# Optimization experiments

Hardware: AMD Instinct MI355X
Metric: run time of the kernel (lower is better)

## Reference

```python
import jax, jax.numpy as jnp
import numpy as np

C = 512

def setup_inputs() -> dict:
    key = jax.random.key(0)
    ks = jax.random.split(key, 7)
    x = jax.random.normal(ks[0], (4, C, 64, 64), dtype=jnp.float32)
    s = 1.0 / np.sqrt(C)
    f_w = jax.random.normal(ks[1], (C // 2, C), dtype=jnp.float32) * s
    f_b = jax.random.normal(ks[2], (C // 2,), dtype=jnp.float32) * 0.01
    g_w = jax.random.normal(ks[3], (C // 2, C), dtype=jnp.float32) * s
    g_b = jax.random.normal(ks[4], (C // 2,), dtype=jnp.float32) * 0.01
    h_w = jax.random.normal(ks[5], (C, C), dtype=jnp.float32) * s
    h_b = jax.random.normal(ks[6], (C,), dtype=jnp.float32) * 0.01
    return {"x": x, "f_w": f_w, "f_b": f_b, "g_w": g_w, "g_b": g_b, "h_w": h_w, "h_b": h_b}

def reference(x, f_w, f_b, g_w, g_b, h_w, h_b):
    B, Cc, H, W = x.shape
    N = H * W
    xf = x.reshape(B, Cc, N)  # hw_flatten
    # 1x1 convs are channel GEMMs: [B,Cout,N]
    f = jnp.einsum('oc,bcn->bon', f_w, xf) + f_b[None, :, None]
    g = jnp.einsum('oc,bcn->bon', g_w, xf) + g_b[None, :, None]
    h = jnp.einsum('oc,bcn->bon', h_w, xf) + h_b[None, :, None]
    # energy[b,i,j] = sum_k f[b,k,i] * g[b,k,j]
    energy = jnp.einsum('bki,bkj->bij', f, g)
    attention = jax.nn.softmax(energy, axis=-1)
    # ret[b,c,i] = sum_j h[b,c,j] * attention[b,i,j]
    ret = jnp.einsum('bcj,bij->bci', h, attention)
    return ret.reshape(B, Cc, H, W)
```

## Files before the change

kernel.cpp:

```cpp
#include <hip/hip_runtime.h>


#define NPIX 4096
#define CIN  512

typedef _Float16 f16x4 __attribute__((ext_vector_type(4)));
typedef _Float16 f16x8 __attribute__((ext_vector_type(8)));
typedef float    f32x4 __attribute__((ext_vector_type(4)));
typedef float    f32x16 __attribute__((ext_vector_type(16)));

#define MFMA16(a, b, c) __builtin_amdgcn_mfma_f32_16x16x16f16(a, b, c, 0, 0, 0)
#define MFMA32(a, b, c) __builtin_amdgcn_mfma_f32_32x32x16_f16(a, b, c, 0, 0, 0)

__device__ __forceinline__ void gld_lds16(const void* g, void* l) {
    __builtin_amdgcn_global_load_lds(
        (const __attribute__((address_space(1))) unsigned int*)g,
        (__attribute__((address_space(3))) unsigned int*)l, 16, 0, 0);
}

__global__ __launch_bounds__(256) void proj_kernel(
    const float* __restrict__ x,
    const float* __restrict__ f_w, const float* __restrict__ f_b,
    const float* __restrict__ g_w, const float* __restrict__ g_b,
    const float* __restrict__ h_w, const float* __restrict__ h_b,
    _Float16* __restrict__ qw, _Float16* __restrict__ kw,
    _Float16* __restrict__ vw)
{
    const int b  = blockIdx.z;
    const int n0 = blockIdx.x * 64;
    const int o0 = blockIdx.y * 64;

    const float* wsrc; const float* bsrc;
    if (o0 < 256)      { wsrc = f_w + (size_t)o0 * CIN;         bsrc = f_b + o0; }
    else if (o0 < 512) { wsrc = g_w + (size_t)(o0 - 256) * CIN; bsrc = g_b + (o0 - 256); }
    else               { wsrc = h_w + (size_t)(o0 - 512) * CIN; bsrc = h_b + (o0 - 512); }

    __shared__ _Float16 Wt[64][40];
    __shared__ _Float16 Xt[64][40];

    const int t = threadIdx.x;
    const int lane = t & 63, wv = t >> 6;
    const int wm = wv >> 1, wn = wv & 1;
    const int gi = lane >> 4, li = lane & 15;

    f32x4 acc[2][2];
    #pragma unroll
    for (int i = 0; i < 2; ++i)
        #pragma unroll
        for (int j = 0; j < 2; ++j) acc[i][j] = f32x4{0.f, 0.f, 0.f, 0.f};

    for (int kk = 0; kk < CIN; kk += 32) {
        {
            const int r = t >> 2, c8 = (t & 3) * 8;
            const float* p = wsrc + (size_t)r * CIN + kk + c8;
            const float4 v0 = *(const float4*)p;
            const float4 v1 = *(const float4*)(p + 4);
            _Float16* d = &Wt[r][c8];
            d[0] = (_Float16)v0.x; d[1] = (_Float16)v0.y;
            d[2] = (_Float16)v0.z; d[3] = (_Float16)v0.w;
            d[4] = (_Float16)v1.x; d[5] = (_Float16)v1.y;
            d[6] = (_Float16)v1.z; d[7] = (_Float16)v1.w;
        }
        {
            const int c = t >> 3, n8 = (t & 7) * 8;
            const float* p = x + ((size_t)b * CIN + kk + c) * NPIX + n0 + n8;
            const float4 v0 = *(const float4*)p;
            const float4 v1 = *(const float4*)(p + 4);
            Xt[n8 + 0][c] = (_Float16)v0.x; Xt[n8 + 1][c] = (_Float16)v0.y;
            Xt[n8 + 2][c] = (_Float16)v0.z; Xt[n8 + 3][c] = (_Float16)v0.w;
            Xt[n8 + 4][c] = (_Float16)v1.x; Xt[n8 + 5][c] = (_Float16)v1.y;
            Xt[n8 + 6][c] = (_Float16)v1.z; Xt[n8 + 7][c] = (_Float16)v1.w;
        }
        __syncthreads();
        #pragma unroll
        for (int kh = 0; kh < 2; ++kh) {
            const int ko = kh * 16 + gi * 4;
            f16x4 a0 = *(const f16x4*)&Wt[wm * 32 +      li][ko];
            f16x4 a1 = *(const f16x4*)&Wt[wm * 32 + 16 + li][ko];
            f16x4 b0 = *(const f16x4*)&Xt[wn * 32 +      li][ko];
            f16x4 b1 = *(const f16x4*)&Xt[wn * 32 + 16 + li][ko];
            acc[0][0] = MFMA16(a0, b0, acc[0][0]);
            acc[0][1] = MFMA16(a0, b1, acc[0][1]);
            acc[1][0] = MFMA16(a1, b0, acc[1][0]);
            acc[1][1] = MFMA16(a1, b1, acc[1][1]);
        }
        __syncthreads();
    }

    #pragma unroll
    for (int mf = 0; mf < 2; ++mf)
        #pragma unroll
        for (int nf = 0; nf < 2; ++nf) {
            const int obase = o0 + wm * 32 + mf * 16 + gi * 4;
            const int n     = n0 + wn * 32 + nf * 16 + li;
            const int brel  = wm * 32 + mf * 16 + gi * 4;
            float v[4];
            #pragma unroll
            for (int r = 0; r < 4; ++r) v[r] = acc[mf][nf][r] + bsrc[brel + r];
            if (o0 < 512) {
                _Float16* dst = (o0 < 256) ? qw : kw;
                const int kb  = (o0 < 256) ? obase : (obase - 256);
                f16x4 pk;
                pk[0] = (_Float16)v[0]; pk[1] = (_Float16)v[1];
                pk[2] = (_Float16)v[2]; pk[3] = (_Float16)v[3];
                *(f16x4*)&dst[((size_t)b * NPIX + n) * 256 + kb] = pk;
            } else {
                #pragma unroll
                for (int r = 0; r < 4; ++r)
                    vw[((size_t)b * CIN + (obase - 512 + r)) * NPIX + n] =
                        (_Float16)v[r];
            }
        }
}

__global__ __launch_bounds__(512, 2) void attn_kernel(
    const _Float16* __restrict__ qw, const _Float16* __restrict__ kw,
    const _Float16* __restrict__ vw,
    _Float16* __restrict__ opart, float* __restrict__ stats)
{
    const int bid = blockIdx.x;
    const int xcd = bid & 7;
    const int jh = xcd & 1, b = xcd >> 1;
    const int rb = bid >> 3;
    const int t = threadIdx.x, l = t & 63, wv = t >> 6;
    const int li = l & 31, g = l >> 5;
    const int rg = wv >> 1, ch = wv & 1;
    const int i_row = rb * 128 + rg * 32 + li;

    __shared__ char Kt[2][16384];
    __shared__ char Vt[2][512 * 72];

    f16x8 qf[16];
    {
        const _Float16* qb = qw + ((size_t)b * NPIX + i_row) * 256 + 8 * g;
        #pragma unroll
        for (int ks = 0; ks < 16; ++ks) qf[ks] = *(const f16x8*)(qb + ks * 16);
    }

    f32x16 oacc[8];
    #pragma unroll
    for (int i = 0; i < 8; ++i)
        #pragma unroll
        for (int e = 0; e < 16; ++e) oacc[i][e] = 0.f;
    float m_run = -__builtin_inff();
    float l_run = 0.f;

    f16x8 vreg[4];

    auto stageK = [&](int buf, int j0) {
        #pragma unroll
        for (int q = 0; q < 2; ++q) {
            const int slot = q * 512 + t;
            const int row  = slot >> 5;
            const int colb = (slot & 31) * 16;
            const char* src =
                (const char*)(kw + ((size_t)b * NPIX + j0 + row) * 256) +
                (colb ^ ((row & 31) << 4));
            gld_lds16(src, Kt[buf] + slot * 16);
        }
    };
    auto loadV = [&](int j0) {
        #pragma unroll
        for (int q = 0; q < 4; ++q) {
            const int c  = q * 128 + (t >> 2);
            const int jj = (t & 3) * 8;
            vreg[q] = *(const f16x8*)(vw + ((size_t)b * CIN + c) * NPIX + j0 + jj);
        }
    };
    auto writeV = [&](int buf) {
        #pragma unroll
        for (int q = 0; q < 4; ++q) {
            const int c = q * 128 + (t >> 2);
            char* d = Vt[buf] + c * 72 + (t & 3) * 16;
            *(f16x4*)d       = *(f16x4*)&vreg[q];
            *(f16x4*)(d + 8) = *((f16x4*)&vreg[q] + 1);
        }
    };

    const int jbase = jh * 2048;
    stageK(0, jbase);
    loadV(jbase);
    writeV(0);
    __syncthreads();

    for (int it = 0; it < 64; ++it) {
        const int cur = it & 1;
        if (it < 63) {
            stageK(cur ^ 1, jbase + (it + 1) * 32);
            loadV(jbase + (it + 1) * 32);
        }

        f32x16 s;
        #pragma unroll
        for (int e = 0; e < 16; ++e) s[e] = 0.f;
        {
            const char* kr = Kt[cur] + li * 512;
            const int sw = (li & 31) << 4;
            #pragma unroll
            for (int ks = 0; ks < 16; ++ks) {
                f16x8 kf = *(const f16x8*)(kr + ((ks * 32 + 16 * g) ^ sw));
                s = MFMA32(kf, qf[ks], s);
            }
        }

        if (it < 63) writeV(cur ^ 1);

        float tmax = s[0];
        #pragma unroll
        for (int e = 1; e < 16; ++e) tmax = fmaxf(tmax, s[e]);
        tmax = fmaxf(tmax, __shfl_xor(tmax, 32));
        if (!__all((int)(tmax - m_run <= 5.f))) {
            const float mnew = fmaxf(m_run, tmax);
            const float sc = __expf(m_run - mnew);
            #pragma unroll
            for (int ct = 0; ct < 8; ++ct)
                #pragma unroll
                for (int e = 0; e < 16; ++e) oacc[ct][e] *= sc;
            l_run *= sc;
            m_run = mnew;
        }
        float p[16];
        float rs = 0.f;
        #pragma unroll
        for (int e = 0; e < 16; ++e) { p[e] = __expf(s[e] - m_run); rs += p[e]; }
        rs += __shfl_xor(rs, 32);
        l_run += rs;

        f16x8 pa0, pa1;
        #pragma unroll
        for (int e = 0; e < 8; ++e) {
            pa0[e] = (_Float16)p[e];
            pa1[e] = (_Float16)p[8 + e];
        }

        #pragma unroll
        for (int ct = 0; ct < 8; ++ct) {
            const int c = ch * 256 + ct * 32 + li;
            const char* vr = Vt[cur] + c * 72;
            f16x8 va;
            *(f16x4*)&va       = *(const f16x4*)(vr + 8 * g);
            *((f16x4*)&va + 1) = *(const f16x4*)(vr + 16 + 8 * g);
            oacc[ct] = MFMA32(va, pa0, oacc[ct]);
            f16x8 vc;
            *(f16x4*)&vc       = *(const f16x4*)(vr + 32 + 8 * g);
            *((f16x4*)&vc + 1) = *(const f16x4*)(vr + 48 + 8 * g);
            oacc[ct] = MFMA32(vc, pa1, oacc[ct]);
        }
        __syncthreads();
    }

    const size_t ob = (size_t)(jh * 4 + b) * CIN * NPIX;
    #pragma unroll
    for (int ct = 0; ct < 8; ++ct)
        #pragma unroll
        for (int r = 0; r < 16; ++r) {
            const int c = ch * 256 + ct * 32 + (r & 3) + 8 * (r >> 2) + 4 * g;
            opart[ob + (size_t)c * NPIX + i_row] = (_Float16)oacc[ct][r];
        }
    if (ch == 0 && g == 0) {
        const size_t idx = ((size_t)(jh * 4 + b) * NPIX + i_row) * 2;
        stats[idx]     = m_run;
        stats[idx + 1] = l_run;
    }
}

__global__ __launch_bounds__(256) void combine_kernel(
    const _Float16* __restrict__ opart, const float* __restrict__ stats,
    float* __restrict__ out)
{
    const int b  = blockIdx.y;
    const int i0 = blockIdx.x * 64;
    const int t  = threadIdx.x;

    __shared__ float a0s[64], a1s[64];
    if (t < 64) {
        const int i = i0 + t;
        const size_t r0 = ((size_t)b * NPIX + i) * 2;
        const size_t r1 = ((size_t)(4 + b) * NPIX + i) * 2;
        const float m0 = stats[r0], l0 = stats[r0 + 1];
        const float m1 = stats[r1], l1 = stats[r1 + 1];
        const float M  = fmaxf(m0, m1);
        const float w0 = __expf(m0 - M), w1 = __expf(m1 - M);
        const float inv = 1.0f / (l0 * w0 + l1 * w1);
        a0s[t] = w0 * inv;
        a1s[t] = w1 * inv;
    }
    __syncthreads();

    const int ci = t >> 3;
    const int ii = (t & 7) * 8;
    #pragma unroll 4
    for (int pp = 0; pp < 16; ++pp) {
        const int c = pp * 32 + ci;
        const _Float16* p0 = opart + ((size_t)b * CIN + c) * NPIX + i0 + ii;
        const _Float16* p1 = opart + ((size_t)(4 + b) * CIN + c) * NPIX + i0 + ii;
        const f16x8 x0 = *(const f16x8*)p0;
        const f16x8 x1 = *(const f16x8*)p1;
        float* dst = out + ((size_t)b * CIN + c) * NPIX + i0 + ii;
        float4 o0, o1;
        o0.x = a0s[ii + 0] * (float)x0[0] + a1s[ii + 0] * (float)x1[0];
        o0.y = a0s[ii + 1] * (float)x0[1] + a1s[ii + 1] * (float)x1[1];
        o0.z = a0s[ii + 2] * (float)x0[2] + a1s[ii + 2] * (float)x1[2];
        o0.w = a0s[ii + 3] * (float)x0[3] + a1s[ii + 3] * (float)x1[3];
        o1.x = a0s[ii + 4] * (float)x0[4] + a1s[ii + 4] * (float)x1[4];
        o1.y = a0s[ii + 5] * (float)x0[5] + a1s[ii + 5] * (float)x1[5];
        o1.z = a0s[ii + 6] * (float)x0[6] + a1s[ii + 6] * (float)x1[6];
        o1.w = a0s[ii + 7] * (float)x0[7] + a1s[ii + 7] * (float)x1[7];
        *(float4*)dst       = o0;
        *(float4*)(dst + 4) = o1;
    }
}

extern "C" void kernel_launch(void* const* d_in, const int* in_sizes, int n_in,
                              void* d_out, int out_size, void* d_ws,
                              size_t ws_size, hipStream_t stream)
{
    const float* x   = (const float*)d_in[0];
    const float* f_w = (const float*)d_in[1];
    const float* f_b = (const float*)d_in[2];
    const float* g_w = (const float*)d_in[3];
    const float* g_b = (const float*)d_in[4];
    const float* h_w = (const float*)d_in[5];
    const float* h_b = (const float*)d_in[6];
    float* out = (float*)d_out;

    _Float16* qw = (_Float16*)d_ws;
    _Float16* kw = qw + (size_t)4 * NPIX * 256;
    _Float16* vw = kw + (size_t)4 * NPIX * 256;
    _Float16* op = vw + (size_t)4 * CIN * NPIX;
    float* stats = (float*)(op + (size_t)2 * 4 * CIN * NPIX);

    proj_kernel<<<dim3(64, 16, 4), 256, 0, stream>>>(
        x, f_w, f_b, g_w, g_b, h_w, h_b, qw, kw, vw);
    attn_kernel<<<dim3(256), 512, 0, stream>>>(qw, kw, vw, op, stats);
    combine_kernel<<<dim3(64, 4), 256, 0, stream>>>(op, stats, out);
}
```

Before: 286.6 us.

## Compute scores once per row group and share probabilities through LDS

In the attention kernel, the two channel-half waves that cover the same query rows used to compute the same QK^T scores and softmax independently. Now only the ch==0 wave does that work. It writes the fp16 probabilities and its rescale factor to a double-buffered LDS area, and the ch==1 wave reads them after an extra barrier. The V staging write moves to the end of the iteration, and setprio hints are placed around the MFMA blocks. In the projection kernel, the LDS stores become vectorized f16x8 writes and x is read with a transposed access pattern. The change removes duplicated MFMA and exp work in exchange for an extra barrier per iteration, more LDS use, and an uneven workload between the two waves.

```diff
diff --git a/kernel.cpp b/kernel.cpp
--- a/kernel.cpp
+++ b/kernel.cpp
@@ -55,21 +55,22 @@
             const float* p = wsrc + (size_t)r * CIN + kk + c8;
             const float4 v0 = *(const float4*)p;
             const float4 v1 = *(const float4*)(p + 4);
-            _Float16* d = &Wt[r][c8];
-            d[0] = (_Float16)v0.x; d[1] = (_Float16)v0.y;
-            d[2] = (_Float16)v0.z; d[3] = (_Float16)v0.w;
-            d[4] = (_Float16)v1.x; d[5] = (_Float16)v1.y;
-            d[6] = (_Float16)v1.z; d[7] = (_Float16)v1.w;
+            f16x8 w8;
+            w8[0] = (_Float16)v0.x; w8[1] = (_Float16)v0.y;
+            w8[2] = (_Float16)v0.z; w8[3] = (_Float16)v0.w;
+            w8[4] = (_Float16)v1.x; w8[5] = (_Float16)v1.y;
+            w8[6] = (_Float16)v1.z; w8[7] = (_Float16)v1.w;
+            *(f16x8*)&Wt[r][c8] = w8;
         }
         {
-            const int c = t >> 3, n8 = (t & 7) * 8;
-            const float* p = x + ((size_t)b * CIN + kk + c) * NPIX + n0 + n8;
-            const float4 v0 = *(const float4*)p;
-            const float4 v1 = *(const float4*)(p + 4);
-            Xt[n8 + 0][c] = (_Float16)v0.x; Xt[n8 + 1][c] = (_Float16)v0.y;
-            Xt[n8 + 2][c] = (_Float16)v0.z; Xt[n8 + 3][c] = (_Float16)v0.w;
-            Xt[n8 + 4][c] = (_Float16)v1.x; Xt[n8 + 5][c] = (_Float16)v1.y;
-            Xt[n8 + 6][c] = (_Float16)v1.z; Xt[n8 + 7][c] = (_Float16)v1.w;
+            const int cb = (t >> 6) * 8;
+            const int nl = t & 63;
+            f16x8 xv;
+            #pragma unroll
+            for (int e = 0; e < 8; ++e)
+                xv[e] = (_Float16)x[((size_t)b * CIN + kk + cb + e) * NPIX +
+                                    n0 + nl];
+            *(f16x8*)&Xt[nl][cb] = xv;
         }
         __syncthreads();
         #pragma unroll
@@ -124,14 +125,15 @@
     const int rb = bid >> 3;
     const int t = threadIdx.x, l = t & 63, wv = t >> 6;
     const int li = l & 31, g = l >> 5;
-    const int rg = wv >> 1, ch = wv & 1;
+    const int ch = wv & 1, rg = wv >> 1;
     const int i_row = rb * 128 + rg * 32 + li;
 
     __shared__ char Kt[2][16384];
     __shared__ char Vt[2][512 * 72];
+    __shared__ char Pt[2][4][64 * 48];
 
     f16x8 qf[16];
-    {
+    if (ch == 0) {
         const _Float16* qb = qw + ((size_t)b * NPIX + i_row) * 256 + 8 * g;
         #pragma unroll
         for (int ks = 0; ks < 16; ++ks) qf[ks] = *(const f16x8*)(qb + ks * 16);
@@ -190,49 +192,71 @@
             loadV(jbase + (it + 1) * 32);
         }
 
-        f32x16 s;
-        #pragma unroll
-        for (int e = 0; e < 16; ++e) s[e] = 0.f;
-        {
-            const char* kr = Kt[cur] + li * 512;
-            const int sw = (li & 31) << 4;
-            #pragma unroll
-            for (int ks = 0; ks < 16; ++ks) {
-                f16x8 kf = *(const f16x8*)(kr + ((ks * 32 + 16 * g) ^ sw));
-                s = MFMA32(kf, qf[ks], s);
-            }
-        }
-
-        if (it < 63) writeV(cur ^ 1);
-
-        float tmax = s[0];
-        #pragma unroll
-        for (int e = 1; e < 16; ++e) tmax = fmaxf(tmax, s[e]);
-        tmax = fmaxf(tmax, __shfl_xor(tmax, 32));
-        if (!__all((int)(tmax - m_run <= 5.f))) {
-            const float mnew = fmaxf(m_run, tmax);
-            const float sc = __expf(m_run - mnew);
-            #pragma unroll
-            for (int ct = 0; ct < 8; ++ct)
+        f16x8 pa0, pa1;
+        if (ch == 0) {
+            f32x16 s;
+            #pragma unroll
+            for (int e = 0; e < 16; ++e) s[e] = 0.f;
+            {
+                const char* kr = Kt[cur] + li * 512;
+                const int sw = li << 4;
+                __builtin_amdgcn_s_setprio(1);
                 #pragma unroll
-                for (int e = 0; e < 16; ++e) oacc[ct][e] *= sc;
-            l_run *= sc;
-            m_run = mnew;
-        }
-        float p[16];
-        float rs = 0.f;
-        #pragma unroll
-        for (int e = 0; e < 16; ++e) { p[e] = __expf(s[e] - m_run); rs += p[e]; }
-        rs += __shfl_xor(rs, 32);
-        l_run += rs;
-
-        f16x8 pa0, pa1;
-        #pragma unroll
-        for (int e = 0; e < 8; ++e) {
-            pa0[e] = (_Float16)p[e];
-            pa1[e] = (_Float16)p[8 + e];
-        }
-
+                for (int ks = 0; ks < 16; ++ks) {
+                    f16x8 kf = *(const f16x8*)(kr + ((ks * 32 + 16 * g) ^ sw));
+                    s = MFMA32(kf, qf[ks], s);
+                }
+                __builtin_amdgcn_s_setprio(0);
+            }
+
+            float tmax = s[0];
+            #pragma unroll
+            for (int e = 1; e < 16; ++e) tmax = fmaxf(tmax, s[e]);
+            tmax = fmaxf(tmax, __shfl_xor(tmax, 32));
+            float sc_my = 1.0f;
+            if (!__all((int)(tmax - m_run <= 5.f))) {
+                const float mnew = fmaxf(m_run, tmax);
+                sc_my = __expf(m_run - mnew);
+                #pragma unroll
+                for (int ct = 0; ct < 8; ++ct)
+                    #pragma unroll
+                    for (int e = 0; e < 16; ++e) oacc[ct][e] *= sc_my;
+                l_run *= sc_my;
+                m_run = mnew;
+            }
+            float p[16];
+            float rs = 0.f;
+            #pragma unroll
+            for (int e = 0; e < 16; ++e) { p[e] = __expf(s[e] - m_run); rs += p[e]; }
+            rs += __shfl_xor(rs, 32);
+            l_run += rs;
+
+            #pragma unroll
+            for (int e = 0; e < 8; ++e) {
+                pa0[e] = (_Float16)p[e];
+                pa1[e] = (_Float16)p[8 + e];
+            }
+            char* pd = Pt[cur][rg] + l * 48;
+            *(f16x8*)pd        = pa0;
+            *(f16x8*)(pd + 16) = pa1;
+            *(float*)(pd + 32) = sc_my;
+        }
+        __syncthreads();
+
+        if (ch == 1) {
+            const char* ps = Pt[cur][rg] + l * 48;
+            pa0 = *(const f16x8*)ps;
+            pa1 = *(const f16x8*)(ps + 16);
+            const float sc = *(const float*)(ps + 32);
+            if (!__all((int)(sc == 1.0f))) {
+                #pragma unroll
+                for (int ct = 0; ct < 8; ++ct)
+                    #pragma unroll
+                    for (int e = 0; e < 16; ++e) oacc[ct][e] *= sc;
+            }
+        }
+
+        __builtin_amdgcn_s_setprio(1);
         #pragma unroll
         for (int ct = 0; ct < 8; ++ct) {
             const int c = ch * 256 + ct * 32 + li;
@@ -246,7 +270,9 @@
             *((f16x4*)&vc + 1) = *(const f16x4*)(vr + 48 + 8 * g);
             oacc[ct] = MFMA32(vc, pa1, oacc[ct]);
         }
-        __syncthreads();
+        __builtin_amdgcn_s_setprio(0);
+
+        if (it < 63) writeV(cur ^ 1);
     }
 
     const size_t ob = (size_t)(jh * 4 + b) * CIN * NPIX;
```

Result: faster. 235.8 us (-17.7%).
